# Performance work log

Hardware: AMD Instinct MI355X
Metric: run time of the kernel (lower is better)

Reference implementation:

```python
import jax, jax.numpy as jnp
import numpy as np
from jax import lax

CHUNK = 256  # query chunk size (manual tiling block)

def setup_inputs() -> dict:
    key = jax.random.key(0)
    kq, kk, kv = jax.random.split(key, 3)
    shape = (2, 16, 2048, 128)  # [B, H, S, D]
    q = jax.random.normal(kq, shape, dtype=jnp.float32)
    k = jax.random.normal(kk, shape, dtype=jnp.float32)
    v = jax.random.normal(kv, shape, dtype=jnp.float32)
    return {"q": q, "k": k, "v": v}

def reference(q, k, v):
    # Chunked (memory-efficient) exact attention: softmax(QK^T/sqrt(D)) V,
    # computed one query block at a time so the full [S,S] score matrix
    # is never materialized.
    B, H, S, D = q.shape
    scale = jnp.asarray(1.0 / np.sqrt(D), dtype=q.dtype)
    n_chunks = S // CHUNK
    # [n_chunks, B, H, CHUNK, D]
    q_blocks = q.reshape(B, H, n_chunks, CHUNK, D).transpose(2, 0, 1, 3, 4)

    def step(carry, q_blk):
        # scores for this query block vs all keys: [B, H, CHUNK, S]
        s = jnp.einsum('bhqd,bhkd->bhqk', q_blk, k) * scale
        p = jax.nn.softmax(s, axis=-1)
        o = jnp.einsum('bhqk,bhkd->bhqd', p, v)
        return carry, o

    _, out_blocks = lax.scan(step, None, q_blocks)
    # [n_chunks, B, H, CHUNK, D] -> [B, H, S, D]
    out = out_blocks.transpose(1, 2, 0, 3, 4).reshape(B, H, S, D)
    return out
```

## Files before the change

kernel.cpp:

```cpp
#include <hip/hip_runtime.h>
#include <hip/hip_bf16.h>


typedef short short8 __attribute__((ext_vector_type(8)));
typedef float f32x16 __attribute__((ext_vector_type(16)));

#define MFMA32(a, b, c) __builtin_amdgcn_mfma_f32_32x32x16_bf16((a), (b), (c), 0, 0, 0)

#if __has_builtin(__builtin_amdgcn_exp2f)
#define EXP2(x) __builtin_amdgcn_exp2f(x)
#else
#define EXP2(x) exp2f(x)
#endif

constexpr int Dh  = 128;
constexpr int S_  = 2048;
constexpr int KVB = 64;
constexpr int NT  = S_ / KVB;
constexpr int WAVES = 4;
constexpr int QBLK  = 128;

__device__ __forceinline__ short f2bf(float f) {
    union { float f; unsigned u; } x; x.f = f;
    unsigned r = x.u + 0x7fffu + ((x.u >> 16) & 1u);
    return (short)(r >> 16);
}

__device__ __forceinline__ unsigned pkbf(float lo, float hi) {
    unsigned r;
    asm("v_cvt_pk_bf16_f32 %0, %1, %2" : "=v"(r) : "v"(lo), "v"(hi));
    return r;
}

__device__ __forceinline__ void pswap(unsigned &a, unsigned &b) {
    asm("v_permlane32_swap_b32 %0, %1" : "+v"(a), "+v"(b));
}

__device__ __forceinline__ void gload16(const void* g, void* l) {
    __builtin_amdgcn_global_load_lds(
        (const __attribute__((address_space(1))) unsigned int*)g,
        (__attribute__((address_space(3))) unsigned int*)l, 16, 0, 0);
}

__global__ __launch_bounds__(256) void prep_k(const float* __restrict__ K,
                                              short* __restrict__ Kz) {
    int idx = blockIdx.x * 256 + threadIdx.x;
    int b   = idx & 15;
    int s   = (idx >> 4) & (S_ - 1);
    int sb  = b ^ (s & 15);
    const float* src = K + (size_t)(idx >> 4) * Dh + sb * 8;
    float4 f0 = ((const float4*)src)[0];
    float4 f1 = ((const float4*)src)[1];
    short8 o;
    o[0] = f2bf(f0.x); o[1] = f2bf(f0.y); o[2] = f2bf(f0.z); o[3] = f2bf(f0.w);
    o[4] = f2bf(f1.x); o[5] = f2bf(f1.y); o[6] = f2bf(f1.z); o[7] = f2bf(f1.w);
    *(short8*)(Kz + (size_t)idx * 8) = o;
}

__global__ __launch_bounds__(256) void prep_v(const float* __restrict__ V,
                                              short* __restrict__ Vt) {
    __shared__ short tr[64][72];
    int bid = blockIdx.x;
    int dg = bid & 1, seg = (bid >> 1) & 31, bh = bid >> 6;
    int t = threadIdx.x;
    int s = t >> 2, d0 = (t & 3) * 16;
    const float* src = V + (size_t)(bh * S_ + seg * 64 + s) * Dh + dg * 64 + d0;
    #pragma unroll
    for (int i = 0; i < 16; i += 4) {
        float4 f = *(const float4*)(src + i);
        tr[d0 + i + 0][s] = f2bf(f.x); tr[d0 + i + 1][s] = f2bf(f.y);
        tr[d0 + i + 2][s] = f2bf(f.z); tr[d0 + i + 3][s] = f2bf(f.w);
    }
    __syncthreads();
    int d = t >> 2, j0 = (t & 3) * 2;
    size_t ob = ((size_t)(bh * 32 + seg) * 128 + dg * 64 + d) * 64;
    #pragma unroll
    for (int jj = 0; jj < 2; ++jj) {
        int j = j0 + jj;
        int sj = (j ^ (d & 7)) * 8;
        short8 val = *(const short8*)&tr[d][sj];
        *(short8*)(Vt + ob + j * 8) = val;
    }
}

__global__ __launch_bounds__(256, 2)
void mea_fwd5(const float* __restrict__ Qg, const short* __restrict__ Kz,
              const short* __restrict__ Vt, float* __restrict__ Og, int nqt) {
    __shared__ __align__(16) short k0[KVB * Dh], k1[KVB * Dh];
    __shared__ __align__(16) short v0[Dh * KVB], v1[Dh * KVB];
    __shared__ float bc_lds[WAVES][32];

    const int bid = blockIdx.x;
    const int cpx = (int)gridDim.x >> 3;
    const int swz = (bid & 7) * cpx + (bid >> 3);
    const int qt  = swz % nqt;
    const int bh  = swz / nqt;

    const int tid  = threadIdx.x;
    const int w    = tid >> 6;
    const int lane = tid & 63;
    const int l31  = lane & 31;
    const int hi   = lane >> 5;

    const size_t base = (size_t)bh * S_ * Dh;
    const int    qrow = qt * QBLK + w * 32 + l31;
    const float  QSC  = 0.08838834764831845f * 1.4426950408889634f;

    short8 qf[8];
    {
        const float* qp = Qg + base + (size_t)qrow * Dh;
        #pragma unroll
        for (int kc = 0; kc < 8; ++kc) {
            const float4 f0 = *(const float4*)(qp + kc * 16 + hi * 8);
            const float4 f1 = *(const float4*)(qp + kc * 16 + hi * 8 + 4);
            short8 a;
            a[0] = f2bf(f0.x * QSC); a[1] = f2bf(f0.y * QSC);
            a[2] = f2bf(f0.z * QSC); a[3] = f2bf(f0.w * QSC);
            a[4] = f2bf(f1.x * QSC); a[5] = f2bf(f1.y * QSC);
            a[6] = f2bf(f1.z * QSC); a[7] = f2bf(f1.w * QSC);
            qf[kc] = a;
        }
    }

    f32x16 oacc[4];
    #pragma unroll
    for (int dt = 0; dt < 4; ++dt)
        #pragma unroll
        for (int r = 0; r < 16; ++r) oacc[dt][r] = 0.f;
    float mrun = -1e30f, lpart = 0.f;

    const short* kt0 = Kz + base;
    const short* vt0 = Vt + base;

    auto STAGE = [&](short* kl, short* vl, int t) {
        const short* ks = kt0 + (size_t)t * (KVB * Dh);
        const short* vs = vt0 + (size_t)t * (Dh * KVB);
        #pragma unroll
        for (int i = 0; i < 4; ++i) {
            const int ou = (i * 4 + w) * 512;
            gload16(ks + ou + lane * 8, kl + ou);
            gload16(vs + ou + lane * 8, vl + ou);
        }
    };

    auto COMPUTE = [&](const short* kl, const short* vl) {
        f32x16 sa, sb;
        #pragma unroll
        for (int r = 0; r < 16; ++r) { sa[r] = 0.f; sb[r] = 0.f; }
        __builtin_amdgcn_s_setprio(1);
        #pragma unroll
        for (int kc = 0; kc < 8; ++kc) {
            const int go = (((kc * 2 + hi) ^ (l31 & 15)) * 8);
            const short8 a0 = *(const short8*)&kl[l31 * Dh + go];
            const short8 a1 = *(const short8*)&kl[(32 + l31) * Dh + go];
            sa = MFMA32(a0, qf[kc], sa);
            sb = MFMA32(a1, qf[kc], sb);
        }
        __builtin_amdgcn_s_setprio(0);

        float mxl = sa[0];
        #pragma unroll
        for (int r = 1; r < 16; ++r) mxl = fmaxf(mxl, sa[r]);
        #pragma unroll
        for (int r = 0; r < 16; ++r) mxl = fmaxf(mxl, sb[r]);
        if (__any(mxl > mrun + 8.0f)) {
            float mo   = fmaxf(mxl, __shfl_xor(mxl, 32));
            float mnew = fmaxf(mrun, mo);
            float rc   = EXP2(mrun - mnew);
            mrun = mnew;
            lpart *= rc;
            if (!hi) bc_lds[w][l31] = rc;
            #pragma unroll
            for (int m = 0; m < 4; ++m) {
                const float4 rcv = *(const float4*)&bc_lds[w][m * 8 + 4 * hi];
                #pragma unroll
                for (int t2 = 0; t2 < 4; ++t2) {
                    const float f = (&rcv.x)[t2];
                    #pragma unroll
                    for (int dt = 0; dt < 4; ++dt) oacc[dt][m * 4 + t2] *= f;
                }
            }
        }

        f32x16 pa, pb;
        float s0 = 0.f, s1 = 0.f;
        #pragma unroll
        for (int r = 0; r < 16; ++r) { pa[r] = EXP2(sa[r] - mrun); s0 += pa[r]; }
        #pragma unroll
        for (int r = 0; r < 16; ++r) { pb[r] = EXP2(sb[r] - mrun); s1 += pb[r]; }
        lpart += s0 + s1;

        short8 pf[4];
        {
            #pragma unroll
            for (int kk = 0; kk < 2; ++kk) {
                unsigned a0 = pkbf(pa[kk * 8 + 0], pa[kk * 8 + 1]);
                unsigned a1 = pkbf(pa[kk * 8 + 2], pa[kk * 8 + 3]);
                unsigned b0 = pkbf(pa[kk * 8 + 4], pa[kk * 8 + 5]);
                unsigned b1 = pkbf(pa[kk * 8 + 6], pa[kk * 8 + 7]);
                pswap(a0, b0); pswap(a1, b1);
                unsigned wd[4] = {a0, a1, b0, b1};
                pf[kk] = *(const short8*)wd;
            }
            #pragma unroll
            for (int kk = 0; kk < 2; ++kk) {
                unsigned a0 = pkbf(pb[kk * 8 + 0], pb[kk * 8 + 1]);
                unsigned a1 = pkbf(pb[kk * 8 + 2], pb[kk * 8 + 3]);
                unsigned b0 = pkbf(pb[kk * 8 + 4], pb[kk * 8 + 5]);
                unsigned b1 = pkbf(pb[kk * 8 + 6], pb[kk * 8 + 7]);
                pswap(a0, b0); pswap(a1, b1);
                unsigned wd[4] = {a0, a1, b0, b1};
                pf[2 + kk] = *(const short8*)wd;
            }
        }

        __builtin_amdgcn_s_setprio(1);
        #pragma unroll
        for (int dt = 0; dt < 4; ++dt) {
            #pragma unroll
            for (int ks = 0; ks < 4; ++ks) {
                const short8 bv = *(const short8*)
                    &vl[(dt * 32 + l31) * KVB + (((ks * 2 + hi) ^ (l31 & 7)) * 8)];
                oacc[dt] = MFMA32(pf[ks], bv, oacc[dt]);
            }
        }
        __builtin_amdgcn_s_setprio(0);
    };

    STAGE(k0, v0, 0);
    __syncthreads();
    #pragma unroll 1
    for (int t = 0; t < NT; t += 2) {
        STAGE(k1, v1, t + 1);
        COMPUTE(k0, v0);
        __syncthreads();
        if (t + 2 < NT) STAGE(k0, v0, t + 2);
        COMPUTE(k1, v1);
        __syncthreads();
    }

    {
        const float tot = lpart + __shfl_xor(lpart, 32);
        if (!hi) bc_lds[w][l31] = 1.0f / tot;
    }
    float* op = Og + base;
    #pragma unroll
    for (int m = 0; m < 4; ++m) {
        const float4 li = *(const float4*)&bc_lds[w][m * 8 + 4 * hi];
        #pragma unroll
        for (int t2 = 0; t2 < 4; ++t2) {
            const int row  = m * 8 + 4 * hi + t2;
            const float lf = (&li.x)[t2];
            #pragma unroll
            for (int dt = 0; dt < 4; ++dt)
                op[(size_t)(qt * QBLK + w * 32 + row) * Dh + dt * 32 + l31]
                    = oacc[dt][m * 4 + t2] * lf;
        }
    }
}

typedef float f32x4 __attribute__((ext_vector_type(4)));
#define MFMA16(a, b, c) __builtin_amdgcn_mfma_f32_16x16x32_bf16((a), (b), (c), 0, 0, 0)
constexpr int FKVB = 32;
constexpr int FKP  = 136;
constexpr int FVP  = 40;
constexpr int FPP  = 40;

__global__ __launch_bounds__(256, 2)
void mea_fwd_fb(const float* __restrict__ Qg, const float* __restrict__ Kg,
                const float* __restrict__ Vg, float* __restrict__ Og,
                int S, int nqt) {
    __shared__ __align__(16) short k_lds[FKVB][FKP];
    __shared__ __align__(16) short vT_lds[Dh][FVP];
    __shared__ __align__(16) short p_lds[4][16][FPP];

    const int qt = blockIdx.x % nqt;
    const int bh = blockIdx.x / nqt;
    const int tid = threadIdx.x;
    const int w = tid >> 6, lane = tid & 63;
    const int lr = lane & 15, lg = lane >> 4;
    const size_t base = (size_t)bh * S * Dh;
    const int qrow0 = qt * 64 + w * 16;
    const float scale = 0.08838834764831845f;

    short8 qf[4];
    {
        const float* qp = Qg + base + (size_t)(qrow0 + lr) * Dh;
        #pragma unroll
        for (int kc = 0; kc < 4; ++kc) {
            const float4 f0 = *(const float4*)(qp + kc * 32 + lg * 8);
            const float4 f1 = *(const float4*)(qp + kc * 32 + lg * 8 + 4);
            short8 a;
            a[0] = f2bf(f0.x); a[1] = f2bf(f0.y); a[2] = f2bf(f0.z); a[3] = f2bf(f0.w);
            a[4] = f2bf(f1.x); a[5] = f2bf(f1.y); a[6] = f2bf(f1.z); a[7] = f2bf(f1.w);
            qf[kc] = a;
        }
    }
    f32x4 oacc[8];
    #pragma unroll
    for (int dt = 0; dt < 8; ++dt) oacc[dt] = (f32x4){0.f, 0.f, 0.f, 0.f};
    float mrun[4] = {-1e30f, -1e30f, -1e30f, -1e30f};
    float lrun[4] = {0.f, 0.f, 0.f, 0.f};
    const int sr = tid >> 3, sc = (tid & 7) * 16;

    for (int kv0 = 0; kv0 < S; kv0 += FKVB) {
        {
            const float* kp = Kg + base + (size_t)(kv0 + sr) * Dh + sc;
            const float* vp = Vg + base + (size_t)(kv0 + sr) * Dh + sc;
            short8 pk0, pk1;
            float4 f0 = ((const float4*)kp)[0], f1 = ((const float4*)kp)[1];
            float4 f2 = ((const float4*)kp)[2], f3 = ((const float4*)kp)[3];
            pk0[0] = f2bf(f0.x); pk0[1] = f2bf(f0.y); pk0[2] = f2bf(f0.z); pk0[3] = f2bf(f0.w);
            pk0[4] = f2bf(f1.x); pk0[5] = f2bf(f1.y); pk0[6] = f2bf(f1.z); pk0[7] = f2bf(f1.w);
            pk1[0] = f2bf(f2.x); pk1[1] = f2bf(f2.y); pk1[2] = f2bf(f2.z); pk1[3] = f2bf(f2.w);
            pk1[4] = f2bf(f3.x); pk1[5] = f2bf(f3.y); pk1[6] = f2bf(f3.z); pk1[7] = f2bf(f3.w);
            *(short8*)&k_lds[sr][sc] = pk0;
            *(short8*)&k_lds[sr][sc + 8] = pk1;
            #pragma unroll
            for (int i = 0; i < 4; ++i) {
                float4 f = ((const float4*)vp)[i];
                vT_lds[sc + 4 * i + 0][sr] = f2bf(f.x);
                vT_lds[sc + 4 * i + 1][sr] = f2bf(f.y);
                vT_lds[sc + 4 * i + 2][sr] = f2bf(f.z);
                vT_lds[sc + 4 * i + 3][sr] = f2bf(f.w);
            }
        }
        __syncthreads();
        f32x4 s0 = (f32x4){0.f,0.f,0.f,0.f}, s1 = (f32x4){0.f,0.f,0.f,0.f};
        #pragma unroll
        for (int kc = 0; kc < 4; ++kc) {
            short8 b0 = *(const short8*)&k_lds[lr][kc * 32 + lg * 8];
            short8 b1 = *(const short8*)&k_lds[16 + lr][kc * 32 + lg * 8];
            s0 = MFMA16(qf[kc], b0, s0);
            s1 = MFMA16(qf[kc], b1, s1);
        }
        float resc[4];
        #pragma unroll
        for (int r = 0; r < 4; ++r) {
            float mxv = fmaxf(s0[r], s1[r]);
            #pragma unroll
            for (int m = 1; m < 16; m <<= 1) mxv = fmaxf(mxv, __shfl_xor(mxv, m));
            float mnew = fmaxf(mrun[r], mxv * scale);
            float rc = __expf(mrun[r] - mnew);
            mrun[r] = mnew;
            float p0 = __expf(s0[r] * scale - mnew);
            float p1 = __expf(s1[r] * scale - mnew);
            float rs = p0 + p1;
            #pragma unroll
            for (int m = 1; m < 16; m <<= 1) rs += __shfl_xor(rs, m);
            lrun[r] = lrun[r] * rc + rs;
            resc[r] = rc;
            p_lds[w][lg * 4 + r][lr] = f2bf(p0);
            p_lds[w][lg * 4 + r][16 + lr] = f2bf(p1);
        }
        #pragma unroll
        for (int dt = 0; dt < 8; ++dt) {
            f32x4 o = oacc[dt];
            o[0] *= resc[0]; o[1] *= resc[1]; o[2] *= resc[2]; o[3] *= resc[3];
            oacc[dt] = o;
        }
        short8 ap = *(const short8*)&p_lds[w][lr][lg * 8];
        #pragma unroll
        for (int dt = 0; dt < 8; ++dt) {
            short8 bv = *(const short8*)&vT_lds[dt * 16 + lr][lg * 8];
            oacc[dt] = MFMA16(ap, bv, oacc[dt]);
        }
        __syncthreads();
    }
    float inv[4];
    #pragma unroll
    for (int r = 0; r < 4; ++r) inv[r] = 1.0f / lrun[r];
    float* op = Og + base;
    #pragma unroll
    for (int dt = 0; dt < 8; ++dt)
        #pragma unroll
        for (int r = 0; r < 4; ++r)
            op[(size_t)(qrow0 + lg * 4 + r) * Dh + dt * 16 + lr] = oacc[dt][r] * inv[r];
}

extern "C" void kernel_launch(void* const* d_in, const int* in_sizes, int n_in,
                              void* d_out, int out_size, void* d_ws, size_t ws_size,
                              hipStream_t stream) {
    const float* q = (const float*)d_in[0];
    const float* k = (const float*)d_in[1];
    const float* v = (const float*)d_in[2];
    float* o = (float*)d_out;

    const int BH  = in_sizes[0] / (S_ * Dh);
    const int nqt = S_ / QBLK;

    const size_t kz_bytes = (size_t)BH * S_ * Dh * sizeof(short);
    const size_t need = 2 * kz_bytes;

    if (ws_size >= need) {
        short* Kz = (short*)d_ws;
        short* Vt = (short*)((char*)d_ws + kz_bytes);
        hipLaunchKernelGGL(prep_k, dim3(BH * S_ * 16 / 256), dim3(256), 0, stream, k, Kz);
        hipLaunchKernelGGL(prep_v, dim3(BH * (S_ / 64) * 2), dim3(256), 0, stream, v, Vt);
        hipLaunchKernelGGL(mea_fwd5, dim3(BH * nqt), dim3(256), 0, stream, q, Kz, Vt, o, nqt);
    } else {
        hipLaunchKernelGGL(mea_fwd_fb, dim3(BH * (S_ / 64)), dim3(256), 0, stream,
                           q, k, v, o, S_, S_ / 64);
    }
}
```

Measured before the change: 97.32 us.

## Software-pipeline QK of next tile with softmax/PV, triple-buffer LDS, 8 waves

```diff
diff --git a/kernel.cpp b/kernel.cpp
--- a/kernel.cpp
+++ b/kernel.cpp
@@ -17,8 +17,8 @@
 constexpr int S_  = 2048;
 constexpr int KVB = 64;
 constexpr int NT  = S_ / KVB;
-constexpr int WAVES = 4;
-constexpr int QBLK  = 128;
+constexpr int WAVES = 8;
+constexpr int QBLK  = 256;
 
 __device__ __forceinline__ short f2bf(float f) {
     union { float f; unsigned u; } x; x.f = f;
@@ -83,11 +83,11 @@
     }
 }
 
-__global__ __launch_bounds__(256, 2)
-void mea_fwd5(const float* __restrict__ Qg, const short* __restrict__ Kz,
+__global__ __launch_bounds__(512, 2)
+void mea_fwd6(const float* __restrict__ Qg, const short* __restrict__ Kz,
               const short* __restrict__ Vt, float* __restrict__ Og, int nqt) {
-    __shared__ __align__(16) short k0[KVB * Dh], k1[KVB * Dh];
-    __shared__ __align__(16) short v0[Dh * KVB], v1[Dh * KVB];
+    __shared__ __align__(16) short kbuf[3][KVB * Dh];
+    __shared__ __align__(16) short vbuf[3][Dh * KVB];
     __shared__ float bc_lds[WAVES][32];
 
     const int bid = blockIdx.x;
@@ -132,32 +132,36 @@
     const short* kt0 = Kz + base;
     const short* vt0 = Vt + base;
 
+    short *kA = kbuf[0], *kB = kbuf[1], *kC = kbuf[2];
+    short *vA = vbuf[0], *vB = vbuf[1], *vC = vbuf[2];
+
     auto STAGE = [&](short* kl, short* vl, int t) {
         const short* ks = kt0 + (size_t)t * (KVB * Dh);
         const short* vs = vt0 + (size_t)t * (Dh * KVB);
         #pragma unroll
-        for (int i = 0; i < 4; ++i) {
-            const int ou = (i * 4 + w) * 512;
+        for (int i = 0; i < 2; ++i) {
+            const int ou = (i * 8 + w) * 512;
             gload16(ks + ou + lane * 8, kl + ou);
             gload16(vs + ou + lane * 8, vl + ou);
         }
     };
 
-    auto COMPUTE = [&](const short* kl, const short* vl) {
-        f32x16 sa, sb;
-        #pragma unroll
-        for (int r = 0; r < 16; ++r) { sa[r] = 0.f; sb[r] = 0.f; }
+    auto QKSTEP = [&](const short* kl, f32x16& A, f32x16& B) {
+        #pragma unroll
+        for (int r = 0; r < 16; ++r) { A[r] = 0.f; B[r] = 0.f; }
         __builtin_amdgcn_s_setprio(1);
         #pragma unroll
         for (int kc = 0; kc < 8; ++kc) {
             const int go = (((kc * 2 + hi) ^ (l31 & 15)) * 8);
             const short8 a0 = *(const short8*)&kl[l31 * Dh + go];
             const short8 a1 = *(const short8*)&kl[(32 + l31) * Dh + go];
-            sa = MFMA32(a0, qf[kc], sa);
-            sb = MFMA32(a1, qf[kc], sb);
+            A = MFMA32(a0, qf[kc], A);
+            B = MFMA32(a1, qf[kc], B);
         }
         __builtin_amdgcn_s_setprio(0);
-
+    };
+
+    auto SMPACK = [&](f32x16& sa, f32x16& sb, short8* pf) {
         float mxl = sa[0];
         #pragma unroll
         for (int r = 1; r < 16; ++r) mxl = fmaxf(mxl, sa[r]);
@@ -181,7 +185,6 @@
                 }
             }
         }
-
         f32x16 pa, pb;
         float s0 = 0.f, s1 = 0.f;
         #pragma unroll
@@ -189,31 +192,29 @@
         #pragma unroll
         for (int r = 0; r < 16; ++r) { pb[r] = EXP2(sb[r] - mrun); s1 += pb[r]; }
         lpart += s0 + s1;
-
-        short8 pf[4];
-        {
-            #pragma unroll
-            for (int kk = 0; kk < 2; ++kk) {
-                unsigned a0 = pkbf(pa[kk * 8 + 0], pa[kk * 8 + 1]);
-                unsigned a1 = pkbf(pa[kk * 8 + 2], pa[kk * 8 + 3]);
-                unsigned b0 = pkbf(pa[kk * 8 + 4], pa[kk * 8 + 5]);
-                unsigned b1 = pkbf(pa[kk * 8 + 6], pa[kk * 8 + 7]);
-                pswap(a0, b0); pswap(a1, b1);
-                unsigned wd[4] = {a0, a1, b0, b1};
-                pf[kk] = *(const short8*)wd;
-            }
-            #pragma unroll
-            for (int kk = 0; kk < 2; ++kk) {
-                unsigned a0 = pkbf(pb[kk * 8 + 0], pb[kk * 8 + 1]);
-                unsigned a1 = pkbf(pb[kk * 8 + 2], pb[kk * 8 + 3]);
-                unsigned b0 = pkbf(pb[kk * 8 + 4], pb[kk * 8 + 5]);
-                unsigned b1 = pkbf(pb[kk * 8 + 6], pb[kk * 8 + 7]);
-                pswap(a0, b0); pswap(a1, b1);
-                unsigned wd[4] = {a0, a1, b0, b1};
-                pf[2 + kk] = *(const short8*)wd;
-            }
-        }
-
+        #pragma unroll
+        for (int kk = 0; kk < 2; ++kk) {
+            unsigned a0 = pkbf(pa[kk * 8 + 0], pa[kk * 8 + 1]);
+            unsigned a1 = pkbf(pa[kk * 8 + 2], pa[kk * 8 + 3]);
+            unsigned b0 = pkbf(pa[kk * 8 + 4], pa[kk * 8 + 5]);
+            unsigned b1 = pkbf(pa[kk * 8 + 6], pa[kk * 8 + 7]);
+            pswap(a0, b0); pswap(a1, b1);
+            unsigned wd[4] = {a0, a1, b0, b1};
+            pf[kk] = *(const short8*)wd;
+        }
+        #pragma unroll
+        for (int kk = 0; kk < 2; ++kk) {
+            unsigned a0 = pkbf(pb[kk * 8 + 0], pb[kk * 8 + 1]);
+            unsigned a1 = pkbf(pb[kk * 8 + 2], pb[kk * 8 + 3]);
+            unsigned b0 = pkbf(pb[kk * 8 + 4], pb[kk * 8 + 5]);
+            unsigned b1 = pkbf(pb[kk * 8 + 6], pb[kk * 8 + 7]);
+            pswap(a0, b0); pswap(a1, b1);
+            unsigned wd[4] = {a0, a1, b0, b1};
+            pf[2 + kk] = *(const short8*)wd;
+        }
+    };
+
+    auto PVSTEP = [&](const short* vl, const short8* pf) {
         __builtin_amdgcn_s_setprio(1);
         #pragma unroll
         for (int dt = 0; dt < 4; ++dt) {
@@ -227,16 +228,33 @@
         __builtin_amdgcn_s_setprio(0);
     };
 
-    STAGE(k0, v0, 0);
+    auto BODY = [&](int t, f32x16& cA, f32x16& cB, f32x16& nA, f32x16& nB) {
+        if (t + 2 < NT) STAGE(kC, vC, t + 2);
+        QKSTEP(kB, nA, nB);
+        short8 pf[4];
+        SMPACK(cA, cB, pf);
+        PVSTEP(vA, pf);
+        __syncthreads();
+        short* tk = kA; kA = kB; kB = kC; kC = tk;
+        short* tv = vA; vA = vB; vB = vC; vC = tv;
+    };
+
+    STAGE(kA, vA, 0);
+    STAGE(kB, vB, 1);
     __syncthreads();
+    f32x16 s0A, s0B, s1A, s1B;
+    QKSTEP(kA, s0A, s0B);
+
     #pragma unroll 1
-    for (int t = 0; t < NT; t += 2) {
-        STAGE(k1, v1, t + 1);
-        COMPUTE(k0, v0);
-        __syncthreads();
-        if (t + 2 < NT) STAGE(k0, v0, t + 2);
-        COMPUTE(k1, v1);
-        __syncthreads();
+    for (int kk = 0; kk < 15; ++kk) {
+        BODY(2 * kk,     s0A, s0B, s1A, s1B);
+        BODY(2 * kk + 1, s1A, s1B, s0A, s0B);
+    }
+    BODY(30, s0A, s0B, s1A, s1B);
+    {
+        short8 pf[4];
+        SMPACK(s1A, s1B, pf);
+        PVSTEP(vA, pf);
     }
 
     {
@@ -397,7 +415,7 @@
         short* Vt = (short*)((char*)d_ws + kz_bytes);
         hipLaunchKernelGGL(prep_k, dim3(BH * S_ * 16 / 256), dim3(256), 0, stream, k, Kz);
         hipLaunchKernelGGL(prep_v, dim3(BH * (S_ / 64) * 2), dim3(256), 0, stream, v, Vt);
-        hipLaunchKernelGGL(mea_fwd5, dim3(BH * nqt), dim3(256), 0, stream, q, Kz, Vt, o, nqt);
+        hipLaunchKernelGGL(mea_fwd6, dim3(BH * nqt), dim3(512), 0, stream, q, Kz, Vt, o, nqt);
     } else {
         hipLaunchKernelGGL(mea_fwd_fb, dim3(BH * (S_ / 64)), dim3(256), 0, stream,
                            q, k, v, o, S_, S_ / 64);
```

Result: no change. 95.49 us (-1.9%).

## Load V fragments directly from global in MFMA layout, double Q block per workgroup

Applied to the files above, without the earlier changes.

```diff
diff --git a/kernel.cpp b/kernel.cpp
--- a/kernel.cpp
+++ b/kernel.cpp
@@ -17,8 +17,8 @@
 constexpr int S_  = 2048;
 constexpr int KVB = 64;
 constexpr int NT  = S_ / KVB;
-constexpr int WAVES = 4;
-constexpr int QBLK  = 128;
+constexpr int WAVES = 8;
+constexpr int QBLK  = 256;
 
 __device__ __forceinline__ short f2bf(float f) {
     union { float f; unsigned u; } x; x.f = f;
@@ -42,52 +42,62 @@
         (__attribute__((address_space(3))) unsigned int*)l, 16, 0, 0);
 }
 
-__global__ __launch_bounds__(256) void prep_k(const float* __restrict__ K,
-                                              short* __restrict__ Kz) {
-    int idx = blockIdx.x * 256 + threadIdx.x;
-    int b   = idx & 15;
-    int s   = (idx >> 4) & (S_ - 1);
-    int sb  = b ^ (s & 15);
-    const float* src = K + (size_t)(idx >> 4) * Dh + sb * 8;
-    float4 f0 = ((const float4*)src)[0];
-    float4 f1 = ((const float4*)src)[1];
-    short8 o;
-    o[0] = f2bf(f0.x); o[1] = f2bf(f0.y); o[2] = f2bf(f0.z); o[3] = f2bf(f0.w);
-    o[4] = f2bf(f1.x); o[5] = f2bf(f1.y); o[6] = f2bf(f1.z); o[7] = f2bf(f1.w);
-    *(short8*)(Kz + (size_t)idx * 8) = o;
-}
-
-__global__ __launch_bounds__(256) void prep_v(const float* __restrict__ V,
-                                              short* __restrict__ Vt) {
-    __shared__ short tr[64][72];
-    int bid = blockIdx.x;
-    int dg = bid & 1, seg = (bid >> 1) & 31, bh = bid >> 6;
-    int t = threadIdx.x;
-    int s = t >> 2, d0 = (t & 3) * 16;
-    const float* src = V + (size_t)(bh * S_ + seg * 64 + s) * Dh + dg * 64 + d0;
-    #pragma unroll
-    for (int i = 0; i < 16; i += 4) {
-        float4 f = *(const float4*)(src + i);
-        tr[d0 + i + 0][s] = f2bf(f.x); tr[d0 + i + 1][s] = f2bf(f.y);
-        tr[d0 + i + 2][s] = f2bf(f.z); tr[d0 + i + 3][s] = f2bf(f.w);
-    }
-    __syncthreads();
-    int d = t >> 2, j0 = (t & 3) * 2;
-    size_t ob = ((size_t)(bh * 32 + seg) * 128 + dg * 64 + d) * 64;
-    #pragma unroll
-    for (int jj = 0; jj < 2; ++jj) {
-        int j = j0 + jj;
-        int sj = (j ^ (d & 7)) * 8;
-        short8 val = *(const short8*)&tr[d][sj];
-        *(short8*)(Vt + ob + j * 8) = val;
-    }
-}
-
-__global__ __launch_bounds__(256, 2)
-void mea_fwd5(const float* __restrict__ Qg, const short* __restrict__ Kz,
+__global__ __launch_bounds__(256) void prep_kv(const float* __restrict__ K,
+                                               const float* __restrict__ V,
+                                               short* __restrict__ Kz,
+                                               short* __restrict__ Vt) {
+    __shared__ short tr[64][132];
+    if (blockIdx.x < 4096) {
+        int idx = blockIdx.x * 256 + threadIdx.x;
+        int b   = idx & 15;
+        int s   = (idx >> 4) & (S_ - 1);
+        int sb  = b ^ (s & 15);
+        const float* src = K + (size_t)(idx >> 4) * Dh + sb * 8;
+        float4 f0 = ((const float4*)src)[0];
+        float4 f1 = ((const float4*)src)[1];
+        short8 o;
+        o[0] = f2bf(f0.x); o[1] = f2bf(f0.y); o[2] = f2bf(f0.z); o[3] = f2bf(f0.w);
+        o[4] = f2bf(f1.x); o[5] = f2bf(f1.y); o[6] = f2bf(f1.z); o[7] = f2bf(f1.w);
+        *(short8*)(Kz + (size_t)idx * 8) = o;
+    } else {
+        int bid = blockIdx.x - 4096;
+        int seg = bid & 31, bh = bid >> 5;
+        int t = threadIdx.x;
+        {
+            const int s = t >> 2, d0 = (t & 3) * 32;
+            const float* src = V + ((size_t)(bh * S_ + seg * 64 + s)) * Dh + d0;
+            #pragma unroll
+            for (int i = 0; i < 4; ++i) {
+                float4 f0 = ((const float4*)src)[2 * i];
+                float4 f1 = ((const float4*)src)[2 * i + 1];
+                short8 o;
+                o[0] = f2bf(f0.x); o[1] = f2bf(f0.y); o[2] = f2bf(f0.z); o[3] = f2bf(f0.w);
+                o[4] = f2bf(f1.x); o[5] = f2bf(f1.y); o[6] = f2bf(f1.z); o[7] = f2bf(f1.w);
+                *(short8*)&tr[s][d0 + i * 8] = o;
+            }
+        }
+        __syncthreads();
+        short* outb = Vt + ((size_t)(bh * 32 + seg)) * 8192;
+        #pragma unroll
+        for (int jj = 0; jj < 4; ++jj) {
+            const int j   = (t << 2) | jj;
+            const int dt  = j >> 8;
+            const int ks  = (j >> 6) & 3;
+            const int ln  = j & 63;
+            const int hi2 = ln >> 5, l31 = ln & 31;
+            short8 o;
+            #pragma unroll
+            for (int e = 0; e < 8; ++e)
+                o[e] = tr[ks * 16 + hi2 * 8 + e][dt * 32 + l31];
+            *(short8*)(outb + (size_t)j * 8) = o;
+        }
+    }
+}
+
+__global__ __launch_bounds__(512, 1)
+void mea_fwd9(const float* __restrict__ Qg, const short* __restrict__ Kz,
               const short* __restrict__ Vt, float* __restrict__ Og, int nqt) {
     __shared__ __align__(16) short k0[KVB * Dh], k1[KVB * Dh];
-    __shared__ __align__(16) short v0[Dh * KVB], v1[Dh * KVB];
     __shared__ float bc_lds[WAVES][32];
 
     const int bid = blockIdx.x;
@@ -132,37 +142,42 @@
     const short* kt0 = Kz + base;
     const short* vt0 = Vt + base;
 
-    auto STAGE = [&](short* kl, short* vl, int t) {
+    auto STAGE = [&](short* kl, int t) {
         const short* ks = kt0 + (size_t)t * (KVB * Dh);
-        const short* vs = vt0 + (size_t)t * (Dh * KVB);
-        #pragma unroll
-        for (int i = 0; i < 4; ++i) {
-            const int ou = (i * 4 + w) * 512;
+        #pragma unroll
+        for (int i = 0; i < 2; ++i) {
+            const int ou = (i * 8 + w) * 512;
             gload16(ks + ou + lane * 8, kl + ou);
-            gload16(vs + ou + lane * 8, vl + ou);
         }
     };
 
-    auto COMPUTE = [&](const short* kl, const short* vl) {
-        f32x16 sa, sb;
-        #pragma unroll
-        for (int r = 0; r < 16; ++r) { sa[r] = 0.f; sb[r] = 0.f; }
+#define VLD(vg, dt, ks) (*(const short8*)((vg) + (((dt) * 4 + (ks)) * 64 + lane) * 8))
+
+    auto COMPUTE = [&](const short* kl, int t) {
+        const short* vg = vt0 + (size_t)t * 8192;
+
+        f32x16 SA, SB;
+        #pragma unroll
+        for (int r = 0; r < 16; ++r) { SA[r] = 0.f; SB[r] = 0.f; }
         __builtin_amdgcn_s_setprio(1);
         #pragma unroll
         for (int kc = 0; kc < 8; ++kc) {
             const int go = (((kc * 2 + hi) ^ (l31 & 15)) * 8);
             const short8 a0 = *(const short8*)&kl[l31 * Dh + go];
             const short8 a1 = *(const short8*)&kl[(32 + l31) * Dh + go];
-            sa = MFMA32(a0, qf[kc], sa);
-            sb = MFMA32(a1, qf[kc], sb);
+            SA = MFMA32(a0, qf[kc], SA);
+            SB = MFMA32(a1, qf[kc], SB);
         }
         __builtin_amdgcn_s_setprio(0);
 
-        float mxl = sa[0];
-        #pragma unroll
-        for (int r = 1; r < 16; ++r) mxl = fmaxf(mxl, sa[r]);
-        #pragma unroll
-        for (int r = 0; r < 16; ++r) mxl = fmaxf(mxl, sb[r]);
+        short8 x0 = VLD(vg, 0, 0), x1 = VLD(vg, 0, 1);
+        short8 x2 = VLD(vg, 0, 2), x3 = VLD(vg, 0, 3);
+
+        float mxl = SA[0];
+        #pragma unroll
+        for (int r = 1; r < 16; ++r) mxl = fmaxf(mxl, SA[r]);
+        #pragma unroll
+        for (int r = 0; r < 16; ++r) mxl = fmaxf(mxl, SB[r]);
         if (__any(mxl > mrun + 8.0f)) {
             float mo   = fmaxf(mxl, __shfl_xor(mxl, 32));
             float mnew = fmaxf(mrun, mo);
@@ -182,60 +197,66 @@
             }
         }
 
-        f32x16 pa, pb;
-        float s0 = 0.f, s1 = 0.f;
-        #pragma unroll
-        for (int r = 0; r < 16; ++r) { pa[r] = EXP2(sa[r] - mrun); s0 += pa[r]; }
-        #pragma unroll
-        for (int r = 0; r < 16; ++r) { pb[r] = EXP2(sb[r] - mrun); s1 += pb[r]; }
-        lpart += s0 + s1;
+        float sum = 0.f;
+        #pragma unroll
+        for (int r = 0; r < 16; ++r) { SA[r] = EXP2(SA[r] - mrun); sum += SA[r]; }
+        #pragma unroll
+        for (int r = 0; r < 16; ++r) { SB[r] = EXP2(SB[r] - mrun); sum += SB[r]; }
+        lpart += sum;
 
         short8 pf[4];
-        {
-            #pragma unroll
-            for (int kk = 0; kk < 2; ++kk) {
-                unsigned a0 = pkbf(pa[kk * 8 + 0], pa[kk * 8 + 1]);
-                unsigned a1 = pkbf(pa[kk * 8 + 2], pa[kk * 8 + 3]);
-                unsigned b0 = pkbf(pa[kk * 8 + 4], pa[kk * 8 + 5]);
-                unsigned b1 = pkbf(pa[kk * 8 + 6], pa[kk * 8 + 7]);
-                pswap(a0, b0); pswap(a1, b1);
-                unsigned wd[4] = {a0, a1, b0, b1};
-                pf[kk] = *(const short8*)wd;
-            }
-            #pragma unroll
-            for (int kk = 0; kk < 2; ++kk) {
-                unsigned a0 = pkbf(pb[kk * 8 + 0], pb[kk * 8 + 1]);
-                unsigned a1 = pkbf(pb[kk * 8 + 2], pb[kk * 8 + 3]);
-                unsigned b0 = pkbf(pb[kk * 8 + 4], pb[kk * 8 + 5]);
-                unsigned b1 = pkbf(pb[kk * 8 + 6], pb[kk * 8 + 7]);
-                pswap(a0, b0); pswap(a1, b1);
-                unsigned wd[4] = {a0, a1, b0, b1};
-                pf[2 + kk] = *(const short8*)wd;
-            }
-        }
-
+        #pragma unroll
+        for (int kk = 0; kk < 2; ++kk) {
+            unsigned a0 = pkbf(SA[kk * 8 + 0], SA[kk * 8 + 1]);
+            unsigned a1 = pkbf(SA[kk * 8 + 2], SA[kk * 8 + 3]);
+            unsigned b0 = pkbf(SA[kk * 8 + 4], SA[kk * 8 + 5]);
+            unsigned b1 = pkbf(SA[kk * 8 + 6], SA[kk * 8 + 7]);
+            pswap(a0, b0); pswap(a1, b1);
+            unsigned wd[4] = {a0, a1, b0, b1};
+            pf[kk] = *(const short8*)wd;
+        }
+        #pragma unroll
+        for (int kk = 0; kk < 2; ++kk) {
+            unsigned a0 = pkbf(SB[kk * 8 + 0], SB[kk * 8 + 1]);
+            unsigned a1 = pkbf(SB[kk * 8 + 2], SB[kk * 8 + 3]);
+            unsigned b0 = pkbf(SB[kk * 8 + 4], SB[kk * 8 + 5]);
+            unsigned b1 = pkbf(SB[kk * 8 + 6], SB[kk * 8 + 7]);
+            pswap(a0, b0); pswap(a1, b1);
+            unsigned wd[4] = {a0, a1, b0, b1};
+            pf[2 + kk] = *(const short8*)wd;
+        }
+
+        short8 w0 = VLD(vg, 1, 0), w1 = VLD(vg, 1, 1);
+        short8 w2 = VLD(vg, 1, 2), w3 = VLD(vg, 1, 3);
         __builtin_amdgcn_s_setprio(1);
-        #pragma unroll
-        for (int dt = 0; dt < 4; ++dt) {
-            #pragma unroll
-            for (int ks = 0; ks < 4; ++ks) {
-                const short8 bv = *(const short8*)
-                    &vl[(dt * 32 + l31) * KVB + (((ks * 2 + hi) ^ (l31 & 7)) * 8)];
-                oacc[dt] = MFMA32(pf[ks], bv, oacc[dt]);
-            }
-        }
+        oacc[0] = MFMA32(pf[0], x0, oacc[0]); oacc[0] = MFMA32(pf[1], x1, oacc[0]);
+        oacc[0] = MFMA32(pf[2], x2, oacc[0]); oacc[0] = MFMA32(pf[3], x3, oacc[0]);
+        __builtin_amdgcn_s_setprio(0);
+        x0 = VLD(vg, 2, 0); x1 = VLD(vg, 2, 1);
+        x2 = VLD(vg, 2, 2); x3 = VLD(vg, 2, 3);
+        __builtin_amdgcn_s_setprio(1);
+        oacc[1] = MFMA32(pf[0], w0, oacc[1]); oacc[1] = MFMA32(pf[1], w1, oacc[1]);
+        oacc[1] = MFMA32(pf[2], w2, oacc[1]); oacc[1] = MFMA32(pf[3], w3, oacc[1]);
+        __builtin_amdgcn_s_setprio(0);
+        w0 = VLD(vg, 3, 0); w1 = VLD(vg, 3, 1);
+        w2 = VLD(vg, 3, 2); w3 = VLD(vg, 3, 3);
+        __builtin_amdgcn_s_setprio(1);
+        oacc[2] = MFMA32(pf[0], x0, oacc[2]); oacc[2] = MFMA32(pf[1], x1, oacc[2]);
+        oacc[2] = MFMA32(pf[2], x2, oacc[2]); oacc[2] = MFMA32(pf[3], x3, oacc[2]);
+        oacc[3] = MFMA32(pf[0], w0, oacc[3]); oacc[3] = MFMA32(pf[1], w1, oacc[3]);
+        oacc[3] = MFMA32(pf[2], w2, oacc[3]); oacc[3] = MFMA32(pf[3], w3, oacc[3]);
         __builtin_amdgcn_s_setprio(0);
     };
 
-    STAGE(k0, v0, 0);
+    STAGE(k0, 0);
     __syncthreads();
     #pragma unroll 1
     for (int t = 0; t < NT; t += 2) {
-        STAGE(k1, v1, t + 1);
-        COMPUTE(k0, v0);
+        STAGE(k1, t + 1);
+        COMPUTE(k0, t);
         __syncthreads();
-        if (t + 2 < NT) STAGE(k0, v0, t + 2);
-        COMPUTE(k1, v1);
+        if (t + 2 < NT) STAGE(k0, t + 2);
+        COMPUTE(k1, t + 1);
         __syncthreads();
     }
 
@@ -257,6 +278,7 @@
                     = oacc[dt][m * 4 + t2] * lf;
         }
     }
+#undef VLD
 }
 
 typedef float f32x4 __attribute__((ext_vector_type(4)));
@@ -395,9 +417,10 @@
     if (ws_size >= need) {
         short* Kz = (short*)d_ws;
         short* Vt = (short*)((char*)d_ws + kz_bytes);
-        hipLaunchKernelGGL(prep_k, dim3(BH * S_ * 16 / 256), dim3(256), 0, stream, k, Kz);
-        hipLaunchKernelGGL(prep_v, dim3(BH * (S_ / 64) * 2), dim3(256), 0, stream, v, Vt);
-        hipLaunchKernelGGL(mea_fwd5, dim3(BH * nqt), dim3(256), 0, stream, q, Kz, Vt, o, nqt);
+        hipLaunchKernelGGL(prep_kv, dim3(4096 + BH * 32), dim3(256),
+                           0, stream, k, v, Kz, Vt);
+        hipLaunchKernelGGL(mea_fwd9, dim3(BH * nqt), dim3(512), 0, stream,
+                           q, Kz, Vt, o, nqt);
     } else {
         hipLaunchKernelGGL(mea_fwd_fb, dim3(BH * (S_ / 64)), dim3(256), 0, stream,
                            q, k, v, o, S_, S_ / 64);
```

Result: slower. 99.74 us (+2.5%).
